# Kernel tuning notes

Hardware: AMD Instinct MI355X
Metric: run time of the kernel (lower is better)

The kernel has to match this reference:

```python
import jax, jax.numpy as jnp
import numpy as np

N_NODES = 100000
N_EDGES = 3200000
IN_CH, HID_CH, OUT_CH = 128, 64, 40


def gcn_conv(x, row, col, norm, W, b, n_nodes):
    # linear transform first (PyG GCNConv order), then normalized aggregation
    h = x @ W                                   # [N, out]
    msg = h[row] * norm[:, None]                # [E+N, out] gathered & scaled
    out = jax.ops.segment_sum(msg, col, num_segments=n_nodes)
    return out + b


def setup_inputs() -> dict:
    key = jax.random.key(0)
    k0, k1, k2, k3, k4, k5 = jax.random.split(key, 6)
    x = jax.random.normal(k0, (N_NODES, IN_CH), dtype=jnp.float32)
    edge_index = jax.random.randint(k1, (2, N_EDGES), 0, N_NODES, dtype=jnp.int64)
    # Glorot-ish init for weights
    W1 = jax.random.normal(k2, (IN_CH, HID_CH), dtype=jnp.float32) * (1.0 / np.sqrt(IN_CH))
    b1 = jnp.zeros((HID_CH,), dtype=jnp.float32)
    W2 = jax.random.normal(k3, (HID_CH, OUT_CH), dtype=jnp.float32) * (1.0 / np.sqrt(HID_CH))
    b2 = jnp.zeros((OUT_CH,), dtype=jnp.float32)
    return {"x": x, "edge_index": edge_index, "original_size": N_NODES,
            "W1": W1, "b1": b1, "W2": W2, "b2": b2}


def reference(x, edge_index, original_size, W1, b1, W2, b2):
    n = x.shape[0]
    # add self-loops (GCNConv default)
    loops = jnp.arange(n, dtype=edge_index.dtype)
    row = jnp.concatenate([edge_index[0], loops])   # source
    col = jnp.concatenate([edge_index[1], loops])   # target
    # symmetric normalization: deg over targets with unit edge weights
    deg = jax.ops.segment_sum(jnp.ones_like(col, dtype=x.dtype), col, num_segments=n)
    dinv = jnp.where(deg > 0, jax.lax.rsqrt(deg), 0.0)
    norm = dinv[row] * dinv[col]                    # [E+N]
    h = gcn_conv(x, row, col, norm, W1, b1, n)
    h = gcn_conv(h, row, col, norm, W2, b2, n)
    out = jax.nn.log_softmax(h, axis=1)
    return out[:original_size]
```

## Files before the change

kernel.cpp:

```cpp
#include <hip/hip_runtime.h>
#include <math.h>


#define NN 100000
#define NE 3200000
#define NBUK 391
#define BCAP 8704
#define EPB 16384
#define NBB ((NE + EPB - 1) / EPB)
#define NGB 782


__device__ __forceinline__ unsigned bf16rne(float x) {
  unsigned u = __float_as_uint(x);
  return (u + 0x7fffu + ((u >> 16) & 1u)) >> 16;
}
__device__ __forceinline__ unsigned pack2(float lo, float hi) {
  return bf16rne(lo) | (bf16rne(hi) << 16);
}


__global__ __launch_bounds__(256) void k_bucket_gemm1(const int* __restrict__ ei,
                                                      int* __restrict__ tail,
                                                      unsigned* __restrict__ bucket,
                                                      const float* __restrict__ x,
                                                      const float* __restrict__ W1,
                                                      unsigned* __restrict__ m1b) {
  __shared__ float smem[128 * 64 + 16 * 132];
  const int tid = threadIdx.x;
  const int bx = blockIdx.x;

  if (bx < NBB) {
    int* hist  = (int*)smem;
    int* wbase = hist + NBUK;
    int* loc   = wbase + NBUK;
    const int beg = bx * EPB;
    const int end = min(beg + EPB, NE);
    const int* col = ei + NE;
    for (int b = tid; b < NBUK; b += 256) { hist[b] = 0; loc[b] = 0; }
    __syncthreads();
    for (int e = beg + tid * 4; e < end; e += 1024) {
      int4 c4 = *(const int4*)(col + e);
      atomicAdd(&hist[c4.x >> 8], 1);
      atomicAdd(&hist[c4.y >> 8], 1);
      atomicAdd(&hist[c4.z >> 8], 1);
      atomicAdd(&hist[c4.w >> 8], 1);
    }
    __syncthreads();
    for (int b = tid; b < NBUK; b += 256)
      wbase[b] = atomicAdd(&tail[b], hist[b]);
    __syncthreads();
    for (int e = beg + tid * 4; e < end; e += 1024) {
      int4 c4 = *(const int4*)(col + e);
      int4 r4 = *(const int4*)(ei + e);
      {
        int b = c4.x >> 8;
        unsigned pos = (unsigned)(wbase[b] + atomicAdd(&loc[b], 1));
        if (pos < BCAP) bucket[(size_t)b * BCAP + pos] = ((unsigned)r4.x << 8) | (unsigned)(c4.x & 255);
      }
      {
        int b = c4.y >> 8;
        unsigned pos = (unsigned)(wbase[b] + atomicAdd(&loc[b], 1));
        if (pos < BCAP) bucket[(size_t)b * BCAP + pos] = ((unsigned)r4.y << 8) | (unsigned)(c4.y & 255);
      }
      {
        int b = c4.z >> 8;
        unsigned pos = (unsigned)(wbase[b] + atomicAdd(&loc[b], 1));
        if (pos < BCAP) bucket[(size_t)b * BCAP + pos] = ((unsigned)r4.z << 8) | (unsigned)(c4.z & 255);
      }
      {
        int b = c4.w >> 8;
        unsigned pos = (unsigned)(wbase[b] + atomicAdd(&loc[b], 1));
        if (pos < BCAP) bucket[(size_t)b * BCAP + pos] = ((unsigned)r4.w << 8) | (unsigned)(c4.w & 255);
      }
    }
    return;
  }

  float* ws = smem;
  float* xt = smem + 128 * 64;
  const int row0 = (bx - NBB) * 128;
  {
    const float4* __restrict__ w4 = (const float4*)W1;
    float4* __restrict__ s4 = (float4*)ws;
    for (int i = tid; i < 128 * 16; i += 256) s4[i] = w4[i];
  }
  const int cg = tid & 7;
  const int rg = tid >> 3;
  const int srow = tid & 127;
  const int skh = tid >> 7;
  float acc[4][8];
  #pragma unroll
  for (int i = 0; i < 4; ++i)
    #pragma unroll
    for (int j = 0; j < 8; ++j) acc[i][j] = 0.f;
  const float4* __restrict__ xt4 = (const float4*)xt;
  const float4* __restrict__ ws4 = (const float4*)ws;
  for (int ks = 0; ks < 8; ++ks) {
    __syncthreads();
    {
      int grow = row0 + srow; if (grow > NN - 1) grow = NN - 1;
      const float* xp = x + (size_t)grow * 128 + ks * 16 + skh * 8;
      float4 va = *(const float4*)xp;
      float4 vb = *(const float4*)(xp + 4);
      const int kb = skh * 8;
      xt[(kb + 0) * 132 + srow] = va.x;
      xt[(kb + 1) * 132 + srow] = va.y;
      xt[(kb + 2) * 132 + srow] = va.z;
      xt[(kb + 3) * 132 + srow] = va.w;
      xt[(kb + 4) * 132 + srow] = vb.x;
      xt[(kb + 5) * 132 + srow] = vb.y;
      xt[(kb + 6) * 132 + srow] = vb.z;
      xt[(kb + 7) * 132 + srow] = vb.w;
    }
    __syncthreads();
    #pragma unroll 4
    for (int kk = 0; kk < 16; ++kk) {
      const int k = ks * 16 + kk;
      float4 xv = xt4[kk * 33 + rg];
      float4 wa = ws4[k * 16 + cg * 2];
      float4 wb = ws4[k * 16 + cg * 2 + 1];
      float xr[4] = {xv.x, xv.y, xv.z, xv.w};
      float wc[8] = {wa.x, wa.y, wa.z, wa.w, wb.x, wb.y, wb.z, wb.w};
      #pragma unroll
      for (int i = 0; i < 4; ++i)
        #pragma unroll
        for (int j = 0; j < 8; ++j)
          acc[i][j] = fmaf(xr[i], wc[j], acc[i][j]);
    }
  }
  #pragma unroll
  for (int i = 0; i < 4; ++i) {
    const int row = row0 + rg * 4 + i;
    if (row < NN) {
      uint4 o;
      o.x = pack2(acc[i][0], acc[i][1]);
      o.y = pack2(acc[i][2], acc[i][3]);
      o.z = pack2(acc[i][4], acc[i][5]);
      o.w = pack2(acc[i][6], acc[i][7]);
      ((uint4*)m1b)[row * 8 + cg] = o;
    }
  }
}


__global__ void k_bstart(const int* __restrict__ tail, int* __restrict__ bstart) {
  const int tid = threadIdx.x, lane = tid & 63, wid = tid >> 6;
  int v = (tid < NBUK) ? min(tail[tid], BCAP) : 0;
  int s = v;
  #pragma unroll
  for (int d = 1; d < 64; d <<= 1) { int t = __shfl_up(s, d, 64); if (lane >= d) s += t; }
  __shared__ int wsum[8];
  if (lane == 63) wsum[wid] = s;
  __syncthreads();
  int wpre = 0;
  for (int w = 0; w < wid; ++w) wpre += wsum[w];
  int excl = wpre + s - v;
  if (tid <= NBUK) bstart[tid] = excl;
}


__global__ __launch_bounds__(256) void k_sort(const unsigned* __restrict__ bucket,
                                              const int* __restrict__ tail,
                                              const int* __restrict__ bstart,
                                              int* __restrict__ csr_src,
                                              int* __restrict__ offsets,
                                              float* __restrict__ dinv,
                                              unsigned* __restrict__ m1b) {
  __shared__ int h[256], base_[256], loc[256];
  __shared__ float dv[256];
  __shared__ int sorted[BCAP];
  __shared__ int wsum[4];
  const int b = blockIdx.x;
  const int lo = b << 8;
  const int nc = min(256, NN - lo);
  const int n = min(tail[b], BCAP);
  const int seg0 = bstart[b];
  const unsigned* __restrict__ bk = bucket + (size_t)b * BCAP;
  const int tid = threadIdx.x, lane = tid & 63, wid = tid >> 6;
  h[tid] = 0; loc[tid] = 0;
  __syncthreads();
  int i = tid * 4;
  for (; i + 3 < n; i += 1024) {
    uint4 v = *(const uint4*)(bk + i);
    atomicAdd(&h[v.x & 255u], 1);
    atomicAdd(&h[v.y & 255u], 1);
    atomicAdd(&h[v.z & 255u], 1);
    atomicAdd(&h[v.w & 255u], 1);
  }
  for (; i < n; ++i) atomicAdd(&h[bk[i] & 255u], 1);
  __syncthreads();
  {
    int v = h[tid];
    int s = v;
    #pragma unroll
    for (int d = 1; d < 64; d <<= 1) { int t = __shfl_up(s, d, 64); if (lane >= d) s += t; }
    if (lane == 63) wsum[wid] = s;
    __syncthreads();
    int wpre = 0;
    #pragma unroll
    for (int w = 0; w < 4; ++w) if (w < wid) wpre += wsum[w];
    int excl = wpre + s - v;
    base_[tid] = excl;
    const float dval = rsqrtf((float)(v + 1));
    dv[tid] = dval;
    if (tid < nc) {
      dinv[lo + tid] = dval;
      offsets[lo + tid] = seg0 + excl;
    }
  }
  if (b == 0 && tid == 0) offsets[NN] = bstart[NBUK];
  __syncthreads();
  i = tid * 4;
  for (; i + 3 < n; i += 1024) {
    uint4 v = *(const uint4*)(bk + i);
    { int c = v.x & 255u; sorted[base_[c] + atomicAdd(&loc[c], 1)] = (int)(v.x >> 8); }
    { int c = v.y & 255u; sorted[base_[c] + atomicAdd(&loc[c], 1)] = (int)(v.y >> 8); }
    { int c = v.z & 255u; sorted[base_[c] + atomicAdd(&loc[c], 1)] = (int)(v.z >> 8); }
    { int c = v.w & 255u; sorted[base_[c] + atomicAdd(&loc[c], 1)] = (int)(v.w >> 8); }
  }
  for (; i < n; ++i) {
    unsigned ent = bk[i];
    int c = ent & 255u;
    sorted[base_[c] + atomicAdd(&loc[c], 1)] = (int)(ent >> 8);
  }
  __syncthreads();
  for (int t = tid; t < n; t += 256) csr_src[seg0 + t] = sorted[t];
  {
    const int q = tid & 7;
    uint4* __restrict__ m1rw = (uint4*)m1b;
    for (int r = tid >> 3; r < nc; r += 32) {
      const float d = dv[r];
      uint4 v = m1rw[(size_t)(lo + r) * 8 + q];
      v.x = pack2(__uint_as_float(v.x << 16) * d, __uint_as_float(v.x & 0xffff0000u) * d);
      v.y = pack2(__uint_as_float(v.y << 16) * d, __uint_as_float(v.y & 0xffff0000u) * d);
      v.z = pack2(__uint_as_float(v.z << 16) * d, __uint_as_float(v.z & 0xffff0000u) * d);
      v.w = pack2(__uint_as_float(v.w << 16) * d, __uint_as_float(v.w & 0xffff0000u) * d);
      m1rw[(size_t)(lo + r) * 8 + q] = v;
    }
  }
}


#define ACC8(v, f)                                                   \
  acc[0] = fmaf(__uint_as_float((v).x << 16), (f), acc[0]);          \
  acc[1] = fmaf(__uint_as_float((v).x & 0xffff0000u), (f), acc[1]);  \
  acc[2] = fmaf(__uint_as_float((v).y << 16), (f), acc[2]);          \
  acc[3] = fmaf(__uint_as_float((v).y & 0xffff0000u), (f), acc[3]);  \
  acc[4] = fmaf(__uint_as_float((v).z << 16), (f), acc[4]);          \
  acc[5] = fmaf(__uint_as_float((v).z & 0xffff0000u), (f), acc[5]);  \
  acc[6] = fmaf(__uint_as_float((v).w << 16), (f), acc[6]);          \
  acc[7] = fmaf(__uint_as_float((v).w & 0xffff0000u), (f), acc[7]);


__global__ __launch_bounds__(256) void k_agg1(const unsigned* __restrict__ m1b,
                                              const int* __restrict__ offsets,
                                              const int* __restrict__ csr_src,
                                              const float* __restrict__ dinv,
                                              const float* __restrict__ b1,
                                              float* __restrict__ a1) {
  const int node = blockIdx.x * 4 + (threadIdx.x >> 6);
  const int lane = threadIdx.x & 63;
  const int e = lane >> 3;
  const int q = lane & 7;
  const uint4* __restrict__ m1v = (const uint4*)m1b;
  const int beg = offsets[node], end = offsets[node + 1];
  float acc[8];
  #pragma unroll
  for (int j = 0; j < 8; ++j) acc[j] = 0.f;
  for (int p = beg; p < end; p += 32) {
    const int i0 = p + e, i1 = p + 8 + e, i2 = p + 16 + e, i3 = p + 24 + e;
    const int s0 = csr_src[i0 < end ? i0 : beg];
    const int s1 = csr_src[i1 < end ? i1 : beg];
    const int s2 = csr_src[i2 < end ? i2 : beg];
    const int s3 = csr_src[i3 < end ? i3 : beg];
    const float f0 = (i0 < end) ? 1.f : 0.f;
    const float f1 = (i1 < end) ? 1.f : 0.f;
    const float f2 = (i2 < end) ? 1.f : 0.f;
    const float f3 = (i3 < end) ? 1.f : 0.f;
    uint4 v0 = m1v[s0 * 8 + q];
    uint4 v1 = m1v[s1 * 8 + q];
    uint4 v2 = m1v[s2 * 8 + q];
    uint4 v3 = m1v[s3 * 8 + q];
    ACC8(v0, f0);
    ACC8(v1, f1);
    ACC8(v2, f2);
    ACC8(v3, f3);
  }
  #pragma unroll
  for (int j = 0; j < 8; ++j) {
    acc[j] += __shfl_xor(acc[j], 8, 64);
    acc[j] += __shfl_xor(acc[j], 16, 64);
    acc[j] += __shfl_xor(acc[j], 32, 64);
  }
  if (e == 0) {
    uint4 sv = m1v[node * 8 + q];
    const float d = dinv[node];
    float4 bb0 = ((const float4*)b1)[q * 2];
    float4 bb1 = ((const float4*)b1)[q * 2 + 1];
    float4 o0, o1;
    o0.x = (acc[0] + __uint_as_float(sv.x << 16)) * d + bb0.x;
    o0.y = (acc[1] + __uint_as_float(sv.x & 0xffff0000u)) * d + bb0.y;
    o0.z = (acc[2] + __uint_as_float(sv.y << 16)) * d + bb0.z;
    o0.w = (acc[3] + __uint_as_float(sv.y & 0xffff0000u)) * d + bb0.w;
    o1.x = (acc[4] + __uint_as_float(sv.z << 16)) * d + bb1.x;
    o1.y = (acc[5] + __uint_as_float(sv.z & 0xffff0000u)) * d + bb1.y;
    o1.z = (acc[6] + __uint_as_float(sv.w << 16)) * d + bb1.z;
    o1.w = (acc[7] + __uint_as_float(sv.w & 0xffff0000u)) * d + bb1.w;
    ((float4*)a1)[node * 16 + q * 2] = o0;
    ((float4*)a1)[node * 16 + q * 2 + 1] = o1;
  }
}


__global__ __launch_bounds__(256) void k_gemm2(const float* __restrict__ a1,
                                               const float* __restrict__ W2,
                                               const float* __restrict__ dinv,
                                               unsigned* __restrict__ m2b) {
  __shared__ float ws[64 * 40];
  const int tid = threadIdx.x;
  for (int k = tid; k < 64 * 40; k += 256) ws[k] = W2[k];
  __syncthreads();
  const int idx = blockIdx.x * 256 + tid;
  if (idx >= NN * 20) return;
  const int node = idx / 20;
  const int c0 = (idx - node * 20) * 2;
  const float4* __restrict__ a4 = (const float4*)(a1 + node * 64);
  float acc0 = 0.f, acc1 = 0.f;
  #pragma unroll
  for (int k4 = 0; k4 < 16; ++k4) {
    float4 a = a4[k4];
    acc0 = fmaf(a.x, ws[(k4 * 4 + 0) * 40 + c0], acc0);
    acc1 = fmaf(a.x, ws[(k4 * 4 + 0) * 40 + c0 + 1], acc1);
    acc0 = fmaf(a.y, ws[(k4 * 4 + 1) * 40 + c0], acc0);
    acc1 = fmaf(a.y, ws[(k4 * 4 + 1) * 40 + c0 + 1], acc1);
    acc0 = fmaf(a.z, ws[(k4 * 4 + 2) * 40 + c0], acc0);
    acc1 = fmaf(a.z, ws[(k4 * 4 + 2) * 40 + c0 + 1], acc1);
    acc0 = fmaf(a.w, ws[(k4 * 4 + 3) * 40 + c0], acc0);
    acc1 = fmaf(a.w, ws[(k4 * 4 + 3) * 40 + c0 + 1], acc1);
  }
  const float d = dinv[node];
  m2b[idx] = pack2(acc0 * d, acc1 * d);
}


__device__ __forceinline__ float shfl1(float v, int src) {
  return __shfl(v, src & 63, 64);
}

__global__ __launch_bounds__(256) void k_agg2(const unsigned* __restrict__ m2b,
                                              const int* __restrict__ offsets,
                                              const int* __restrict__ csr_src,
                                              const float* __restrict__ dinv,
                                              const float* __restrict__ b2,
                                              float* __restrict__ out) {
  const int node = blockIdx.x * 4 + (threadIdx.x >> 6);
  const int lane = threadIdx.x & 63;
  const bool act = lane < 60;
  const int e = act ? (lane / 5) : 0;
  const int q = act ? (lane - e * 5) : 0;
  const uint4* __restrict__ m2v = (const uint4*)m2b;
  const int beg = offsets[node], end = offsets[node + 1];
  float acc[8];
  #pragma unroll
  for (int j = 0; j < 8; ++j) acc[j] = 0.f;
  for (int p = beg; p < end; p += 48) {
    const int i0 = p + e, i1 = p + 12 + e, i2 = p + 24 + e, i3 = p + 36 + e;
    const int s0 = csr_src[i0 < end ? i0 : beg];
    const int s1 = csr_src[i1 < end ? i1 : beg];
    const int s2 = csr_src[i2 < end ? i2 : beg];
    const int s3 = csr_src[i3 < end ? i3 : beg];
    const float f0 = (act && i0 < end) ? 1.f : 0.f;
    const float f1 = (act && i1 < end) ? 1.f : 0.f;
    const float f2 = (act && i2 < end) ? 1.f : 0.f;
    const float f3 = (act && i3 < end) ? 1.f : 0.f;
    uint4 v0 = m2v[s0 * 5 + q];
    uint4 v1 = m2v[s1 * 5 + q];
    uint4 v2 = m2v[s2 * 5 + q];
    uint4 v3 = m2v[s3 * 5 + q];
    ACC8(v0, f0);
    ACC8(v1, f1);
    ACC8(v2, f2);
    ACC8(v3, f3);
  }
  #pragma unroll
  for (int j = 0; j < 8; ++j) acc[j] += shfl1(acc[j], lane + 30);
  #pragma unroll
  for (int j = 0; j < 8; ++j) acc[j] += shfl1(acc[j], lane + 15);
  #pragma unroll
  for (int j = 0; j < 8; ++j) {
    float t1 = shfl1(acc[j], lane + 5);
    float t2 = shfl1(acc[j], lane + 10);
    acc[j] += t1 + t2;
  }
  const bool lead = (lane < 5);
  float r[8];
  #pragma unroll
  for (int j = 0; j < 8; ++j) r[j] = 0.f;
  if (lead) {
    uint4 sv = m2v[node * 5 + lane];
    const float d = dinv[node];
    float4 bb0 = ((const float4*)b2)[lane * 2];
    float4 bb1 = ((const float4*)b2)[lane * 2 + 1];
    r[0] = (acc[0] + __uint_as_float(sv.x << 16)) * d + bb0.x;
    r[1] = (acc[1] + __uint_as_float(sv.x & 0xffff0000u)) * d + bb0.y;
    r[2] = (acc[2] + __uint_as_float(sv.y << 16)) * d + bb0.z;
    r[3] = (acc[3] + __uint_as_float(sv.y & 0xffff0000u)) * d + bb0.w;
    r[4] = (acc[4] + __uint_as_float(sv.z << 16)) * d + bb1.x;
    r[5] = (acc[5] + __uint_as_float(sv.z & 0xffff0000u)) * d + bb1.y;
    r[6] = (acc[6] + __uint_as_float(sv.w << 16)) * d + bb1.z;
    r[7] = (acc[7] + __uint_as_float(sv.w & 0xffff0000u)) * d + bb1.w;
  }
  float mx = -INFINITY;
  if (lead) {
    mx = fmaxf(fmaxf(fmaxf(r[0], r[1]), fmaxf(r[2], r[3])),
               fmaxf(fmaxf(r[4], r[5]), fmaxf(r[6], r[7])));
  }
  #pragma unroll
  for (int d = 4; d > 0; d >>= 1) mx = fmaxf(mx, __shfl_xor(mx, d, 8));
  float se = 0.f;
  if (lead) {
    se = __expf(r[0] - mx) + __expf(r[1] - mx) + __expf(r[2] - mx) +
         __expf(r[3] - mx) + __expf(r[4] - mx) + __expf(r[5] - mx) +
         __expf(r[6] - mx) + __expf(r[7] - mx);
  }
  #pragma unroll
  for (int d = 4; d > 0; d >>= 1) se += __shfl_xor(se, d, 8);
  if (lead) {
    const float lse = mx + logf(se);
    float4 o0, o1;
    o0.x = r[0] - lse; o0.y = r[1] - lse; o0.z = r[2] - lse; o0.w = r[3] - lse;
    o1.x = r[4] - lse; o1.y = r[5] - lse; o1.z = r[6] - lse; o1.w = r[7] - lse;
    ((float4*)out)[node * 10 + lane * 2] = o0;
    ((float4*)out)[node * 10 + lane * 2 + 1] = o1;
  }
}


extern "C" void kernel_launch(void* const* d_in, const int* in_sizes, int n_in,
                              void* d_out, int out_size, void* d_ws, size_t ws_size,
                              hipStream_t stream) {
  const float* x   = (const float*)d_in[0];
  const int*   ei  = (const int*)d_in[1];
  const float* W1  = (const float*)d_in[3];
  const float* b1  = (const float*)d_in[4];
  const float* W2  = (const float*)d_in[5];
  const float* b2  = (const float*)d_in[6];
  float*       out = (float*)d_out;

  char* ws = (char*)d_ws;
  int*      tail    = (int*)(ws + 0);
  int*      bstart  = (int*)(ws + (size_t)4 * 1024);
  int*      offsets = (int*)(ws + (size_t)8 * 1024);
  float*    dinv    = (float*)(ws + (size_t)512 * 1024);
  int*      csr_src = (int*)(ws + (size_t)1536 * 1024);
  unsigned* m1b     = (unsigned*)(ws + (size_t)14848 * 1024);
  unsigned* bucket  = (unsigned*)(ws + (size_t)28160 * 1024);
  float*    a1      = (float*)(ws + (size_t)28160 * 1024);
  unsigned* m2b     = m1b;

  hipMemsetAsync(tail, 0, NBUK * 4, stream);
  k_bucket_gemm1<<<NBB + NGB, 256, 0, stream>>>(ei, tail, bucket, x, W1, m1b);
  k_bstart<<<1, 512, 0, stream>>>(tail, bstart);
  k_sort<<<NBUK, 256, 0, stream>>>(bucket, tail, bstart, csr_src, offsets, dinv, m1b);
  k_agg1<<<NN / 4, 256, 0, stream>>>(m1b, offsets, csr_src, dinv, b1, a1);
  k_gemm2<<<(NN * 20 + 255) / 256, 256, 0, stream>>>(a1, W2, dinv, m2b);
  k_agg2<<<NN / 4, 256, 0, stream>>>(m2b, offsets, csr_src, dinv, b2, out);
}
```

Before: 203.2 us.

## Use 512-thread blocks for bucket/GEMM1 and packed FMA in aggregation

The fused bucketing and first-GEMM kernel now runs 512-thread blocks, so each GEMM block covers 256 rows and the bucketing blocks stride twice as far. The transpose tile in shared memory is widened to match. Separately, both aggregation kernels accumulate with inline-asm v_pk_fma_f32 on float2 pairs, aiming to halve the FMA instruction count. Larger blocks use more shared memory and may lower occupancy, and the inline asm limits how the compiler can schedule those instructions.

```diff
diff --git a/kernel.cpp b/kernel.cpp
--- a/kernel.cpp
+++ b/kernel.cpp
@@ -8,7 +8,9 @@
 #define BCAP 8704
 #define EPB 16384
 #define NBB ((NE + EPB - 1) / EPB)
-#define NGB 782
+#define NGB 391
+
+typedef __attribute__((ext_vector_type(2))) float f32x2;
 
 
 __device__ __forceinline__ unsigned bf16rne(float x) {
@@ -20,13 +22,34 @@
 }
 
 
-__global__ __launch_bounds__(256) void k_bucket_gemm1(const int* __restrict__ ei,
+__device__ __forceinline__ void pkfma(f32x2& a, f32x2 v, f32x2 f) {
+  asm("v_pk_fma_f32 %0, %1, %2, %0" : "+v"(a) : "v"(v), "v"(f));
+}
+
+#define ACCP(vv, fp) {                                                      \
+  f32x2 t0, t1, t2, t3;                                                     \
+  t0.x = __uint_as_float((vv).x << 16);                                     \
+  t0.y = __uint_as_float((vv).x & 0xffff0000u);                             \
+  t1.x = __uint_as_float((vv).y << 16);                                     \
+  t1.y = __uint_as_float((vv).y & 0xffff0000u);                             \
+  t2.x = __uint_as_float((vv).z << 16);                                     \
+  t2.y = __uint_as_float((vv).z & 0xffff0000u);                             \
+  t3.x = __uint_as_float((vv).w << 16);                                     \
+  t3.y = __uint_as_float((vv).w & 0xffff0000u);                             \
+  pkfma(acc2[0], t0, fp);                                                   \
+  pkfma(acc2[1], t1, fp);                                                   \
+  pkfma(acc2[2], t2, fp);                                                   \
+  pkfma(acc2[3], t3, fp);                                                   \
+}
+
+
+__global__ __launch_bounds__(512) void k_bucket_gemm1(const int* __restrict__ ei,
                                                       int* __restrict__ tail,
                                                       unsigned* __restrict__ bucket,
                                                       const float* __restrict__ x,
                                                       const float* __restrict__ W1,
                                                       unsigned* __restrict__ m1b) {
-  __shared__ float smem[128 * 64 + 16 * 132];
+  __shared__ float smem[128 * 64 + 16 * 260];
   const int tid = threadIdx.x;
   const int bx = blockIdx.x;
 
@@ -37,9 +60,9 @@
     const int beg = bx * EPB;
     const int end = min(beg + EPB, NE);
     const int* col = ei + NE;
-    for (int b = tid; b < NBUK; b += 256) { hist[b] = 0; loc[b] = 0; }
-    __syncthreads();
-    for (int e = beg + tid * 4; e < end; e += 1024) {
+    for (int b = tid; b < NBUK; b += 512) { hist[b] = 0; loc[b] = 0; }
+    __syncthreads();
+    for (int e = beg + tid * 4; e < end; e += 2048) {
       int4 c4 = *(const int4*)(col + e);
       atomicAdd(&hist[c4.x >> 8], 1);
       atomicAdd(&hist[c4.y >> 8], 1);
@@ -47,10 +70,10 @@
       atomicAdd(&hist[c4.w >> 8], 1);
     }
     __syncthreads();
-    for (int b = tid; b < NBUK; b += 256)
+    for (int b = tid; b < NBUK; b += 512)
       wbase[b] = atomicAdd(&tail[b], hist[b]);
     __syncthreads();
-    for (int e = beg + tid * 4; e < end; e += 1024) {
+    for (int e = beg + tid * 4; e < end; e += 2048) {
       int4 c4 = *(const int4*)(col + e);
       int4 r4 = *(const int4*)(ei + e);
       {
@@ -79,16 +102,16 @@
 
   float* ws = smem;
   float* xt = smem + 128 * 64;
-  const int row0 = (bx - NBB) * 128;
+  const int row0 = (bx - NBB) * 256;
   {
     const float4* __restrict__ w4 = (const float4*)W1;
     float4* __restrict__ s4 = (float4*)ws;
-    for (int i = tid; i < 128 * 16; i += 256) s4[i] = w4[i];
+    for (int i = tid; i < 128 * 16; i += 512) s4[i] = w4[i];
   }
   const int cg = tid & 7;
   const int rg = tid >> 3;
-  const int srow = tid & 127;
-  const int skh = tid >> 7;
+  const int srow = tid & 255;
+  const int skh = tid >> 8;
   float acc[4][8];
   #pragma unroll
   for (int i = 0; i < 4; ++i)
@@ -104,20 +127,20 @@
       float4 va = *(const float4*)xp;
       float4 vb = *(const float4*)(xp + 4);
       const int kb = skh * 8;
-      xt[(kb + 0) * 132 + srow] = va.x;
-      xt[(kb + 1) * 132 + srow] = va.y;
-      xt[(kb + 2) * 132 + srow] = va.z;
-      xt[(kb + 3) * 132 + srow] = va.w;
-      xt[(kb + 4) * 132 + srow] = vb.x;
-      xt[(kb + 5) * 132 + srow] = vb.y;
-      xt[(kb + 6) * 132 + srow] = vb.z;
-      xt[(kb + 7) * 132 + srow] = vb.w;
+      xt[(kb + 0) * 260 + srow] = va.x;
+      xt[(kb + 1) * 260 + srow] = va.y;
+      xt[(kb + 2) * 260 + srow] = va.z;
+      xt[(kb + 3) * 260 + srow] = va.w;
+      xt[(kb + 4) * 260 + srow] = vb.x;
+      xt[(kb + 5) * 260 + srow] = vb.y;
+      xt[(kb + 6) * 260 + srow] = vb.z;
+      xt[(kb + 7) * 260 + srow] = vb.w;
     }
     __syncthreads();
     #pragma unroll 4
     for (int kk = 0; kk < 16; ++kk) {
       const int k = ks * 16 + kk;
-      float4 xv = xt4[kk * 33 + rg];
+      float4 xv = xt4[kk * 65 + rg];
       float4 wa = ws4[k * 16 + cg * 2];
       float4 wb = ws4[k * 16 + cg * 2 + 1];
       float xr[4] = {xv.x, xv.y, xv.z, xv.w};
@@ -242,17 +265,6 @@
 }
 
 
-#define ACC8(v, f)                                                   \
-  acc[0] = fmaf(__uint_as_float((v).x << 16), (f), acc[0]);          \
-  acc[1] = fmaf(__uint_as_float((v).x & 0xffff0000u), (f), acc[1]);  \
-  acc[2] = fmaf(__uint_as_float((v).y << 16), (f), acc[2]);          \
-  acc[3] = fmaf(__uint_as_float((v).y & 0xffff0000u), (f), acc[3]);  \
-  acc[4] = fmaf(__uint_as_float((v).z << 16), (f), acc[4]);          \
-  acc[5] = fmaf(__uint_as_float((v).z & 0xffff0000u), (f), acc[5]);  \
-  acc[6] = fmaf(__uint_as_float((v).w << 16), (f), acc[6]);          \
-  acc[7] = fmaf(__uint_as_float((v).w & 0xffff0000u), (f), acc[7]);
-
-
 __global__ __launch_bounds__(256) void k_agg1(const unsigned* __restrict__ m1b,
                                               const int* __restrict__ offsets,
                                               const int* __restrict__ csr_src,
@@ -265,28 +277,31 @@
   const int q = lane & 7;
   const uint4* __restrict__ m1v = (const uint4*)m1b;
   const int beg = offsets[node], end = offsets[node + 1];
-  float acc[8];
-  #pragma unroll
-  for (int j = 0; j < 8; ++j) acc[j] = 0.f;
+  f32x2 acc2[4];
+  #pragma unroll
+  for (int j = 0; j < 4; ++j) { acc2[j].x = 0.f; acc2[j].y = 0.f; }
   for (int p = beg; p < end; p += 32) {
     const int i0 = p + e, i1 = p + 8 + e, i2 = p + 16 + e, i3 = p + 24 + e;
     const int s0 = csr_src[i0 < end ? i0 : beg];
     const int s1 = csr_src[i1 < end ? i1 : beg];
     const int s2 = csr_src[i2 < end ? i2 : beg];
     const int s3 = csr_src[i3 < end ? i3 : beg];
-    const float f0 = (i0 < end) ? 1.f : 0.f;
-    const float f1 = (i1 < end) ? 1.f : 0.f;
-    const float f2 = (i2 < end) ? 1.f : 0.f;
-    const float f3 = (i3 < end) ? 1.f : 0.f;
+    f32x2 f0; f0.x = f0.y = (i0 < end) ? 1.f : 0.f;
+    f32x2 f1; f1.x = f1.y = (i1 < end) ? 1.f : 0.f;
+    f32x2 f2; f2.x = f2.y = (i2 < end) ? 1.f : 0.f;
+    f32x2 f3; f3.x = f3.y = (i3 < end) ? 1.f : 0.f;
     uint4 v0 = m1v[s0 * 8 + q];
     uint4 v1 = m1v[s1 * 8 + q];
     uint4 v2 = m1v[s2 * 8 + q];
     uint4 v3 = m1v[s3 * 8 + q];
-    ACC8(v0, f0);
-    ACC8(v1, f1);
-    ACC8(v2, f2);
-    ACC8(v3, f3);
-  }
+    ACCP(v0, f0);
+    ACCP(v1, f1);
+    ACCP(v2, f2);
+    ACCP(v3, f3);
+  }
+  float acc[8];
+  acc[0] = acc2[0].x; acc[1] = acc2[0].y; acc[2] = acc2[1].x; acc[3] = acc2[1].y;
+  acc[4] = acc2[2].x; acc[5] = acc2[2].y; acc[6] = acc2[3].x; acc[7] = acc2[3].y;
   #pragma unroll
   for (int j = 0; j < 8; ++j) {
     acc[j] += __shfl_xor(acc[j], 8, 64);
@@ -361,28 +376,31 @@
   const int q = act ? (lane - e * 5) : 0;
   const uint4* __restrict__ m2v = (const uint4*)m2b;
   const int beg = offsets[node], end = offsets[node + 1];
-  float acc[8];
-  #pragma unroll
-  for (int j = 0; j < 8; ++j) acc[j] = 0.f;
+  f32x2 acc2[4];
+  #pragma unroll
+  for (int j = 0; j < 4; ++j) { acc2[j].x = 0.f; acc2[j].y = 0.f; }
   for (int p = beg; p < end; p += 48) {
     const int i0 = p + e, i1 = p + 12 + e, i2 = p + 24 + e, i3 = p + 36 + e;
     const int s0 = csr_src[i0 < end ? i0 : beg];
     const int s1 = csr_src[i1 < end ? i1 : beg];
     const int s2 = csr_src[i2 < end ? i2 : beg];
     const int s3 = csr_src[i3 < end ? i3 : beg];
-    const float f0 = (act && i0 < end) ? 1.f : 0.f;
-    const float f1 = (act && i1 < end) ? 1.f : 0.f;
-    const float f2 = (act && i2 < end) ? 1.f : 0.f;
-    const float f3 = (act && i3 < end) ? 1.f : 0.f;
+    f32x2 f0; f0.x = f0.y = (act && i0 < end) ? 1.f : 0.f;
+    f32x2 f1; f1.x = f1.y = (act && i1 < end) ? 1.f : 0.f;
+    f32x2 f2; f2.x = f2.y = (act && i2 < end) ? 1.f : 0.f;
+    f32x2 f3; f3.x = f3.y = (act && i3 < end) ? 1.f : 0.f;
     uint4 v0 = m2v[s0 * 5 + q];
     uint4 v1 = m2v[s1 * 5 + q];
     uint4 v2 = m2v[s2 * 5 + q];
     uint4 v3 = m2v[s3 * 5 + q];
-    ACC8(v0, f0);
-    ACC8(v1, f1);
-    ACC8(v2, f2);
-    ACC8(v3, f3);
-  }
+    ACCP(v0, f0);
+    ACCP(v1, f1);
+    ACCP(v2, f2);
+    ACCP(v3, f3);
+  }
+  float acc[8];
+  acc[0] = acc2[0].x; acc[1] = acc2[0].y; acc[2] = acc2[1].x; acc[3] = acc2[1].y;
+  acc[4] = acc2[2].x; acc[5] = acc2[2].y; acc[6] = acc2[3].x; acc[7] = acc2[3].y;
   #pragma unroll
   for (int j = 0; j < 8; ++j) acc[j] += shfl1(acc[j], lane + 30);
   #pragma unroll
@@ -460,7 +478,7 @@
   unsigned* m2b     = m1b;
 
   hipMemsetAsync(tail, 0, NBUK * 4, stream);
-  k_bucket_gemm1<<<NBB + NGB, 256, 0, stream>>>(ei, tail, bucket, x, W1, m1b);
+  k_bucket_gemm1<<<NBB + NGB, 512, 0, stream>>>(ei, tail, bucket, x, W1, m1b);
   k_bstart<<<1, 512, 0, stream>>>(tail, bstart);
   k_sort<<<NBUK, 256, 0, stream>>>(bucket, tail, bstart, csr_src, offsets, dinv, m1b);
   k_agg1<<<NN / 4, 256, 0, stream>>>(m1b, offsets, csr_src, dinv, b1, a1);
```

New measurement: 214.1 us. 5.4% more time.
